# Optimization experiments

Measured on AMD Instinct MI355X. Metric: run time of the kernel, lower is better.

Reference implementation:

```python
import jax, jax.numpy as jnp
import numpy as np

T, B, E, H = 256, 8, 512, 32
EXP = 512            # number of expanded (periodic-image) keys
SMOOTH = 20.0        # smooth_factor


def setup_inputs() -> dict:
    key = jax.random.key(0)
    ks = jax.random.split(key, 12)
    s = 1.0 / np.sqrt(E)
    return {
        "query": jax.random.normal(ks[0], (T, B, E), dtype=jnp.float32),
        "outcell_index": jax.random.randint(ks[1], (B, EXP), 0, T),
        "expand_mask": jax.random.bernoulli(ks[2], 0.1, (B, EXP)),
        "key_padding_mask": jax.random.bernoulli(ks[3], 0.1, (B, T)),
        "local_attention_weight": jax.random.uniform(ks[4], (B, T, T + EXP), dtype=jnp.float32),
        "Wq": jax.random.normal(ks[5], (E, E), dtype=jnp.float32) * s,
        "bq": jnp.zeros((E,), dtype=jnp.float32),
        "Wk": jax.random.normal(ks[6], (E, E), dtype=jnp.float32) * s,   # k_bias=False
        "Wv": jax.random.normal(ks[7], (E, E), dtype=jnp.float32) * s,
        "bv": jnp.zeros((E,), dtype=jnp.float32),
        "Wo": jax.random.normal(ks[8], (E, E), dtype=jnp.float32) * s,
        "bo": jnp.zeros((E,), dtype=jnp.float32),
    }


def reference(query, outcell_index, expand_mask, key_padding_mask,
              local_attention_weight, Wq, bq, Wk, Wv, bv, Wo, bo):
    t, b, e = query.shape
    hd = e // H
    # QKV projections (torch Linear: y = x @ W.T + b)
    q = jnp.einsum('tbe,fe->tbf', query, Wq) + bq
    k = jnp.einsum('tbe,fe->tbf', query, Wk)          # no k bias
    v = jnp.einsum('tbe,fe->tbf', query, Wv) + bv
    # PBC gather-expand K/V along the time axis
    oc = outcell_index.T[:, :, None]                  # [EXP, B, 1]
    k = jnp.concatenate([k, jnp.take_along_axis(k, oc, axis=0)], axis=0)  # [S,B,E]
    v = jnp.concatenate([v, jnp.take_along_axis(v, oc, axis=0)], axis=0)
    s_len = k.shape[0]
    # [len, B, E] -> [B, H, len, hd]
    qh = q.reshape(t, b, H, hd).transpose(1, 2, 0, 3)
    kh = k.reshape(s_len, b, H, hd).transpose(1, 2, 0, 3)
    vh = v.reshape(s_len, b, H, hd).transpose(1, 2, 0, 3)
    # NOTE: forward() never applies self.scaling in this path (faithful)
    scores = jnp.einsum('bhtd,bhsd->bhts', qh, kh)    # [B,H,T,S]
    law = local_attention_weight[:, None]             # [B,1,T,S]
    scores = (scores + SMOOTH) * law - SMOOTH         # smooth softmax
    kpm = jnp.concatenate([key_padding_mask, expand_mask], axis=1)  # [B,S]
    scores = jnp.where(kpm[:, None, None, :], -jnp.inf, scores)
    probs = jax.nn.softmax(scores, axis=-1)
    probs = probs * law                               # post-softmax reweight
    attn = jnp.einsum('bhts,bhsd->bhtd', probs, vh)   # [B,H,T,hd]
    attn = attn.transpose(2, 0, 1, 3).reshape(t, b, e)
    return jnp.einsum('tbe,fe->tbf', attn, Wo) + bo
```

## Files before the change

kernel.cpp:

```cpp
#include <hip/hip_runtime.h>
#include <stdint.h>

#define T_ 256
#define B_ 8
#define E_ 512
#define H_ 32
#define HD_ 16
#define EXP_ 512
#define S_ 768
#define M_ 2048
#define SMOOTH_ 20.0f
#define VSTR 776
#define OSTR 20
#define LWSTR 36
#define LOG2E_ 1.44269504f
#define MB0_  (-100.988655f)

typedef __attribute__((ext_vector_type(8)))  short bf16x8;
typedef __attribute__((ext_vector_type(4)))  float f32x4;
typedef __attribute__((ext_vector_type(16))) float f32x16;
typedef __attribute__((ext_vector_type(2)))  unsigned int uint32x2;

__device__ __forceinline__ unsigned int pku(float a, float b)
{
    return ((__float_as_uint(a) + 0x8000u) >> 16) |
           ((__float_as_uint(b) + 0x8000u) & 0xFFFF0000u);
}
__device__ __forceinline__ ushort bf1(float a)
{
    unsigned int u = __float_as_uint(a);
    u = u + 0x7FFFu + ((u >> 16) & 1u);
    return (ushort)(u >> 16);
}

union U16 { uint4 u; bf16x8 v; };

__global__ __launch_bounds__(1024, 4)
void qkv_attn_kernel(const float* __restrict__ X,
                     const float* __restrict__ Wq, const float* __restrict__ Wk,
                     const float* __restrict__ Wv,
                     const float* __restrict__ bq, const float* __restrict__ bv,
                     const float* __restrict__ LAW,
                     const int* __restrict__ kpm, const int* __restrict__ em,
                     const int* __restrict__ oc, ushort* __restrict__ Ab)
{
    __shared__ __align__(16) char raw[134400];
    ushort* Ks  = (ushort*)(raw);
    ushort* Vt  = (ushort*)(raw + 24576);
    ushort* Qi  = (ushort*)(raw + 49408);
    float*  msf = (float*) (raw + 57600);
    float*  LAWf= (float*) (raw + 60672);
    ushort* As  = (ushort*)(raw);
    ushort* Bs  = (ushort*)(raw + 36864);
    float*  Obuf= (float*) (raw);
    float*  Zb  = (float*) (raw + 57600);
    ushort* Ob  = Qi;

    const int bh  = blockIdx.x;
    const int b   = bh & 7;
    const int h   = bh >> 3;
    const int tid = threadIdx.x;
    const int w   = tid >> 6;
    const int l   = tid & 63;

    const int r0 = tid >> 3;
    const int c8 = tid & 7;
    const float* Xc0 = &X[((size_t)r0 * 8 + b) * E_ + c8 * 8];
    const float* Xc1 = Xc0 + (size_t)128 * 8 * E_;

    const int wr = tid >> 3;
    const bool wload = (tid < 384);
    const float* Wsel = (wr < 16) ? Wq : (wr < 32 ? Wk : Wv);
    const float* Wr = &Wsel[((size_t)(h * 16 + (wr & 15))) * E_ + c8 * 8];
    ushort* Bxw = &Bs[wr * 72 + c8 * 8];

    f32x4 acc[3];
#pragma unroll
    for (int m = 0; m < 3; ++m) acc[m] = (f32x4){0.f, 0.f, 0.f, 0.f};

    float4 xa0, xa1, xb0, xb1, wp0, wp1;
    xa0 = *(const float4*)&Xc0[0]; xa1 = *(const float4*)&Xc0[4];
    xb0 = *(const float4*)&Xc1[0]; xb1 = *(const float4*)&Xc1[4];
    if (wload) { wp0 = *(const float4*)&Wr[0]; wp1 = *(const float4*)&Wr[4]; }

    const int ln = l & 15;
    const int lg = l >> 4;

    for (int it = 0; it < 8; ++it) {
        __syncthreads();
        *(uint4*)&As[r0 * 72 + c8 * 8] =
            make_uint4(pku(xa0.x, xa0.y), pku(xa0.z, xa0.w),
                       pku(xa1.x, xa1.y), pku(xa1.z, xa1.w));
        *(uint4*)&As[(r0 + 128) * 72 + c8 * 8] =
            make_uint4(pku(xb0.x, xb0.y), pku(xb0.z, xb0.w),
                       pku(xb1.x, xb1.y), pku(xb1.z, xb1.w));
        if (wload)
            *(uint4*)&Bxw[0] = make_uint4(pku(wp0.x, wp0.y), pku(wp0.z, wp0.w),
                                          pku(wp1.x, wp1.y), pku(wp1.z, wp1.w));
        __syncthreads();
        if (it < 7) {
            Xc0 += 64; Xc1 += 64;
            xa0 = *(const float4*)&Xc0[0]; xa1 = *(const float4*)&Xc0[4];
            xb0 = *(const float4*)&Xc1[0]; xb1 = *(const float4*)&Xc1[4];
            if (wload) { Wr += 64; wp0 = *(const float4*)&Wr[0]; wp1 = *(const float4*)&Wr[4]; }
        }
#pragma unroll
        for (int kb = 0; kb < 2; ++kb) {
            bf16x8 af = *(const bf16x8*)&As[(w * 16 + ln) * 72 + kb * 32 + lg * 8];
#pragma unroll
            for (int m = 0; m < 3; ++m) {
                bf16x8 bfm = *(const bf16x8*)&Bs[(m * 16 + ln) * 72 + kb * 32 + lg * 8];
                acc[m] = __builtin_amdgcn_mfma_f32_16x16x32_bf16(af, bfm, acc[m], 0, 0, 0);
            }
        }
    }

    __syncthreads();

    {
        const float bqv = bq[h * 16 + ln];
        const float bvv = bv[h * 16 + ln];
#pragma unroll
        for (int r = 0; r < 4; ++r) {
            const int t = w * 16 + lg * 4 + r;
            Qi[t * 16 + ln]   = bf1(acc[0][r] + bqv);
            Ks[t * 16 + ln]   = bf1(acc[1][r]);
            Vt[ln * VSTR + t] = bf1(acc[2][r] + bvv);
        }
    }

    const int tq = w & 7;
    const int sh = w >> 3;
    const int i0 = sh * 12;
    const int iend = i0 + 12;
    float* lws = &LAWf[w * 32 * LWSTR];
    const int srow = l >> 1;
    const int scol = (l & 1) * 16;
    const float* gl = &LAW[((size_t)b * T_ + tq * 32 + srow) * S_ + scol];

    float4 g0 = *(const float4*)&gl[i0 * 32 + 0];
    float4 g1 = *(const float4*)&gl[i0 * 32 + 4];
    float4 g2 = *(const float4*)&gl[i0 * 32 + 8];
    float4 g3 = *(const float4*)&gl[i0 * 32 + 12];
    *(float4*)&lws[srow * LWSTR + scol + 0]  = g0;
    *(float4*)&lws[srow * LWSTR + scol + 4]  = g1;
    *(float4*)&lws[srow * LWSTR + scol + 8]  = g2;
    *(float4*)&lws[srow * LWSTR + scol + 12] = g3;
    g0 = *(const float4*)&gl[(i0 + 1) * 32 + 0];
    g1 = *(const float4*)&gl[(i0 + 1) * 32 + 4];
    g2 = *(const float4*)&gl[(i0 + 1) * 32 + 8];
    g3 = *(const float4*)&gl[(i0 + 1) * 32 + 12];

    __syncthreads();

    if (tid < 512) {
        const int j   = tid;
        const int src = oc[b * EXP_ + j];
        uint4 k0 = *(const uint4*)&Ks[src * 16];
        uint4 k1 = *(const uint4*)&Ks[src * 16 + 8];
        *(uint4*)&Ks[(T_ + j) * 16]     = k0;
        *(uint4*)&Ks[(T_ + j) * 16 + 8] = k1;
    } else {
        const int j   = tid - 512;
        const int src = oc[b * EXP_ + j];
#pragma unroll
        for (int d = 0; d < 16; ++d)
            Vt[d * VSTR + T_ + j] = Vt[d * VSTR + src];
    }
    if (tid < 768) {
        const int s = tid;
        const int m = (s < T_) ? kpm[b * T_ + s] : em[b * EXP_ + (s - T_)];
        msf[s] = m ? -1.0e5f : MB0_;
    }
    __syncthreads();

    const int slane = l & 31;
    const int hi    = l >> 5;

    bf16x8 qf = *(const bf16x8*)&Qi[(tq * 32 + slane) * 16 + hi * 8];

    const f32x16 zero16 = {0.f,0.f,0.f,0.f,0.f,0.f,0.f,0.f,
                           0.f,0.f,0.f,0.f,0.f,0.f,0.f,0.f};
    f32x16 oacc = zero16;
    float z = 0.f;

    for (int i = i0; i < iend; ++i) {
        bf16x8 kf = *(const bf16x8*)&Ks[(i * 32 + slane) * 16 + hi * 8];
        f32x16 sc = __builtin_amdgcn_mfma_f32_32x32x16_bf16(kf, qf, zero16, 0, 0, 0);

#pragma unroll
        for (int ks = 0; ks < 2; ++ks) {
            float pp[8];
#pragma unroll
            for (int gi = 0; gi < 2; ++gi) {
                const int g = 2 * ks + gi;
                const float4 lw4 = *(const float4*)&lws[slane * LWSTR + g * 8 + 4 * hi];
                const float4 mb4 = *(const float4*)&msf[i * 32 + g * 8 + 4 * hi];
                const float lwa[4] = {lw4.x, lw4.y, lw4.z, lw4.w};
                const float mba[4] = {mb4.x, mb4.y, mb4.z, mb4.w};
#pragma unroll
                for (int c = 0; c < 4; ++c) {
                    const float lwv = lwa[c];
                    const float lwK = lwv * LOG2E_;
                    const float arg = __builtin_fmaf(sc[8 * ks + 4 * gi + c], lwK,
                                      __builtin_fmaf(lwK, SMOOTH_, mba[c]));
                    const float e = __builtin_amdgcn_exp2f(arg);
                    z += e;
                    pp[4 * gi + c] = e * lwv;
                }
            }
            const unsigned int cA0 = pku(pp[0], pp[1]);
            const unsigned int cA2 = pku(pp[2], pp[3]);
            const unsigned int cB0 = pku(pp[4], pp[5]);
            const unsigned int cB2 = pku(pp[6], pp[7]);
            uint32x2 s0 = __builtin_amdgcn_permlane32_swap(cA0, cB0, false, false);
            uint32x2 s1 = __builtin_amdgcn_permlane32_swap(cA2, cB2, false, false);
            U16 u;
            u.u = make_uint4(s0.x, s1.x, s0.y, s1.y);
            bf16x8 vf = *(const bf16x8*)&Vt[(l & 15) * VSTR + i * 32 + ks * 16 + hi * 8];
            oacc = __builtin_amdgcn_mfma_f32_32x32x16_bf16(u.v, vf, oacc, 0, 0, 0);
        }

        if (i + 1 < iend) {
            *(float4*)&lws[srow * LWSTR + scol + 0]  = g0;
            *(float4*)&lws[srow * LWSTR + scol + 4]  = g1;
            *(float4*)&lws[srow * LWSTR + scol + 8]  = g2;
            *(float4*)&lws[srow * LWSTR + scol + 12] = g3;
            if (i + 2 < iend) {
                g0 = *(const float4*)&gl[(i + 2) * 32 + 0];
                g1 = *(const float4*)&gl[(i + 2) * 32 + 4];
                g2 = *(const float4*)&gl[(i + 2) * 32 + 8];
                g3 = *(const float4*)&gl[(i + 2) * 32 + 12];
            }
        }
    }

    z += __shfl_xor(z, 32);

    __syncthreads();

    if (l < 32) Zb[sh * 256 + tq * 32 + l] = z;

    const int dl = l & 15;
    const bool dok = (l & 31) < 16;
    if (sh == 1 && dok) {
#pragma unroll
        for (int r = 0; r < 16; ++r) {
            const int t = tq * 32 + (r & 3) + 8 * (r >> 2) + 4 * hi;
            Obuf[t * OSTR + dl] = oacc[r];
        }
    }
    __syncthreads();

    if (sh == 0 && dok) {
#pragma unroll
        for (int r = 0; r < 16; ++r) {
            const int t = tq * 32 + (r & 3) + 8 * (r >> 2) + 4 * hi;
            const float Zt  = Zb[t] + Zb[256 + t];
            const float inv = (Zt > 0.f) ? 1.f / Zt : 0.f;
            const float ov  = (oacc[r] + Obuf[t * OSTR + dl]) * inv;
            Ob[t * 16 + dl] = bf1(ov);
        }
    }
    __syncthreads();

    {
        const int t  = tid >> 2;
        const int q4 = tid & 3;
        *(uint2*)&Ab[((size_t)(t * 8 + b)) * E_ + h * 16 + q4 * 4] =
            *(const uint2*)&Ob[t * 16 + q4 * 4];
    }
}

__global__ __launch_bounds__(256, 2)
void out_gemm(const ushort* __restrict__ Ab, const float* __restrict__ Wo,
              const float* __restrict__ bo, float* __restrict__ dst)
{
    __shared__ __align__(16) ushort sbuf[96 * 136];
    ushort* As = sbuf;
    ushort* Bs = sbuf + 32 * 136;

    const int n0 = blockIdx.x * 64;
    const int m0 = blockIdx.y * 32;

    const int tid = threadIdx.x;
    const int arow = tid >> 3;
    const int acol = (tid & 7) * 16;
    const int brow = tid >> 2;
    const int bcol = (tid & 3) * 32;

    const ushort* Ap = &Ab[(size_t)(m0 + arow) * E_ + acol];
    const float*  Wp = &Wo[(size_t)(n0 + brow) * E_ + bcol];

    f32x4 acc[2];
    acc[0] = (f32x4){0.f, 0.f, 0.f, 0.f};
    acc[1] = (f32x4){0.f, 0.f, 0.f, 0.f};

    uint4  ha0 = *(const uint4*)&Ap[0];
    uint4  ha1 = *(const uint4*)&Ap[8];
    float4 f0 = *(const float4*)&Wp[0];
    float4 f1 = *(const float4*)&Wp[4];
    float4 f2 = *(const float4*)&Wp[8];
    float4 f3 = *(const float4*)&Wp[12];
    float4 f4 = *(const float4*)&Wp[16];
    float4 f5 = *(const float4*)&Wp[20];
    float4 f6 = *(const float4*)&Wp[24];
    float4 f7 = *(const float4*)&Wp[28];

    const int l  = tid & 63;
    const int w  = tid >> 6;
    const int wm = w & 1;
    const int wn = w >> 1;
    const int lq = l >> 4;
    const int ln = l & 15;

    for (int it = 0; it < 4; ++it) {
        __syncthreads();
        *(uint4*)&As[arow * 136 + acol]     = ha0;
        *(uint4*)&As[arow * 136 + acol + 8] = ha1;
        *(uint4*)&Bs[brow * 136 + bcol]      = make_uint4(pku(f0.x, f0.y), pku(f0.z, f0.w),
                                                          pku(f1.x, f1.y), pku(f1.z, f1.w));
        *(uint4*)&Bs[brow * 136 + bcol + 8]  = make_uint4(pku(f2.x, f2.y), pku(f2.z, f2.w),
                                                          pku(f3.x, f3.y), pku(f3.z, f3.w));
        *(uint4*)&Bs[brow * 136 + bcol + 16] = make_uint4(pku(f4.x, f4.y), pku(f4.z, f4.w),
                                                          pku(f5.x, f5.y), pku(f5.z, f5.w));
        *(uint4*)&Bs[brow * 136 + bcol + 24] = make_uint4(pku(f6.x, f6.y), pku(f6.z, f6.w),
                                                          pku(f7.x, f7.y), pku(f7.z, f7.w));
        __syncthreads();
        if (it < 3) {
            Ap += 128; Wp += 128;
            ha0 = *(const uint4*)&Ap[0];
            ha1 = *(const uint4*)&Ap[8];
            f0 = *(const float4*)&Wp[0];
            f1 = *(const float4*)&Wp[4];
            f2 = *(const float4*)&Wp[8];
            f3 = *(const float4*)&Wp[12];
            f4 = *(const float4*)&Wp[16];
            f5 = *(const float4*)&Wp[20];
            f6 = *(const float4*)&Wp[24];
            f7 = *(const float4*)&Wp[28];
        }
#pragma unroll
        for (int kb = 0; kb < 4; ++kb) {
            bf16x8 af  = *(const bf16x8*)&As[(wm * 16 + ln) * 136 + kb * 32 + lq * 8];
            bf16x8 bv0 = *(const bf16x8*)&Bs[(wn * 32 + ln) * 136 + kb * 32 + lq * 8];
            bf16x8 bv1 = *(const bf16x8*)&Bs[(wn * 32 + 16 + ln) * 136 + kb * 32 + lq * 8];
            acc[0] = __builtin_amdgcn_mfma_f32_16x16x32_bf16(af, bv0, acc[0], 0, 0, 0);
            acc[1] = __builtin_amdgcn_mfma_f32_16x16x32_bf16(af, bv1, acc[1], 0, 0, 0);
        }
    }

    const float bo0 = bo[n0 + wn * 32 + ln];
    const float bo1 = bo[n0 + wn * 32 + 16 + ln];

    __syncthreads();
    float* Lf = (float*)sbuf;
#pragma unroll
    for (int j = 0; j < 2; ++j) {
        const float bb = j ? bo1 : bo0;
        const f32x4 a = acc[j];
#pragma unroll
        for (int r = 0; r < 4; ++r)
            Lf[(wm * 16 + lq * 4 + r) * 68 + wn * 32 + j * 16 + ln] = a[r] + bb;
    }
    __syncthreads();

    {
        const int orow = tid >> 3;
        const int oc8  = (tid & 7) * 8;
        float* dp = &dst[(size_t)(m0 + orow) * E_ + n0 + oc8];
        float4 v0 = *(const float4*)&Lf[orow * 68 + oc8];
        float4 v1 = *(const float4*)&Lf[orow * 68 + oc8 + 4];
        *(float4*)&dp[0] = v0;
        *(float4*)&dp[4] = v1;
    }
}

extern "C" void kernel_launch(void* const* d_in, const int* in_sizes, int n_in,
                              void* d_out, int out_size, void* d_ws, size_t ws_size,
                              hipStream_t stream)
{
    const float* query = (const float*)d_in[0];
    const int*   oc    = (const int*)d_in[1];
    const int*   em    = (const int*)d_in[2];
    const int*   kpm   = (const int*)d_in[3];
    const float* law   = (const float*)d_in[4];
    const float* Wq    = (const float*)d_in[5];
    const float* bq    = (const float*)d_in[6];
    const float* Wk    = (const float*)d_in[7];
    const float* Wv    = (const float*)d_in[8];
    const float* bv    = (const float*)d_in[9];
    const float* Wo    = (const float*)d_in[10];
    const float* bo    = (const float*)d_in[11];
    float* out = (float*)d_out;

    ushort* Ab = (ushort*)d_ws;

    qkv_attn_kernel<<<B_ * H_, 1024, 0, stream>>>(query, Wq, Wk, Wv, bq, bv,
                                                  law, kpm, em, oc, Ab);

    dim3 go(E_ / 64, M_ / 32, 1);
    out_gemm<<<go, 256, 0, stream>>>(Ab, Wo, bo, out);
}
```

Measured before the change: 125.3 us.

## Double-buffer QKV GEMM, load LAW directly to registers, pad K rows, use hardware bf16 convert

The QKV projection loop now alternates between two LDS buffers, which removes one barrier per iteration. Local attention weights are read straight from global memory into registers with a one-step prefetch, so the LDS staging buffer for them is gone and shared memory shrinks from about 134KB to about 88KB. K and Q rows are padded to stride 20 to reduce bank conflicts and read with split 8-byte loads. The next K fragment, V and the mask are prefetched, and softmax sums are split into four partial accumulators. Pack-to-bf16 now uses the v_cvt_pk_bf16_f32 instruction, which rounds to nearest-even, so results may differ slightly from the old truncating pack.

```diff
diff --git a/kernel.cpp b/kernel.cpp
--- a/kernel.cpp
+++ b/kernel.cpp
@@ -10,9 +10,9 @@
 #define S_ 768
 #define M_ 2048
 #define SMOOTH_ 20.0f
+#define KSTR 20
 #define VSTR 776
 #define OSTR 20
-#define LWSTR 36
 #define LOG2E_ 1.44269504f
 #define MB0_  (-100.988655f)
 
@@ -21,10 +21,11 @@
 typedef __attribute__((ext_vector_type(16))) float f32x16;
 typedef __attribute__((ext_vector_type(2)))  unsigned int uint32x2;
 
-__device__ __forceinline__ unsigned int pku(float a, float b)
-{
-    return ((__float_as_uint(a) + 0x8000u) >> 16) |
-           ((__float_as_uint(b) + 0x8000u) & 0xFFFF0000u);
+__device__ __forceinline__ unsigned int cvtpk(float a, float b)
+{
+    unsigned int r;
+    asm("v_cvt_pk_bf16_f32 %0, %1, %2" : "=v"(r) : "v"(a), "v"(b));
+    return r;
 }
 __device__ __forceinline__ ushort bf1(float a)
 {
@@ -34,6 +35,16 @@
 }
 
 union U16 { uint4 u; bf16x8 v; };
+union U8x2 { uint2 p[2]; bf16x8 v; };
+
+__device__ __forceinline__ bf16x8 ld20(const ushort* base, int row, int hi)
+{
+    U8x2 u;
+    const ushort* p = &base[row * KSTR + hi * 8];
+    u.p[0] = *(const uint2*)(p);
+    u.p[1] = *(const uint2*)(p + 4);
+    return u.v;
+}
 
 __global__ __launch_bounds__(1024, 4)
 void qkv_attn_kernel(const float* __restrict__ X,
@@ -44,16 +55,13 @@
                      const int* __restrict__ kpm, const int* __restrict__ em,
                      const int* __restrict__ oc, ushort* __restrict__ Ab)
 {
-    __shared__ __align__(16) char raw[134400];
+    __shared__ __align__(16) char raw[87552];
     ushort* Ks  = (ushort*)(raw);
-    ushort* Vt  = (ushort*)(raw + 24576);
-    ushort* Qi  = (ushort*)(raw + 49408);
-    float*  msf = (float*) (raw + 57600);
-    float*  LAWf= (float*) (raw + 60672);
-    ushort* As  = (ushort*)(raw);
-    ushort* Bs  = (ushort*)(raw + 36864);
+    ushort* Vt  = (ushort*)(raw + 30720);
+    ushort* Qi  = (ushort*)(raw + 55552);
+    float*  msf = (float*) (raw + 65792);
     float*  Obuf= (float*) (raw);
-    float*  Zb  = (float*) (raw + 57600);
+    float*  Zb  = (float*) (raw + 65792);
     ushort* Ob  = Qi;
 
     const int bh  = blockIdx.x;
@@ -72,7 +80,6 @@
     const bool wload = (tid < 384);
     const float* Wsel = (wr < 16) ? Wq : (wr < 32 ? Wk : Wv);
     const float* Wr = &Wsel[((size_t)(h * 16 + (wr & 15))) * E_ + c8 * 8];
-    ushort* Bxw = &Bs[wr * 72 + c8 * 8];
 
     f32x4 acc[3];
 #pragma unroll
@@ -87,16 +94,18 @@
     const int lg = l >> 4;
 
     for (int it = 0; it < 8; ++it) {
-        __syncthreads();
-        *(uint4*)&As[r0 * 72 + c8 * 8] =
-            make_uint4(pku(xa0.x, xa0.y), pku(xa0.z, xa0.w),
-                       pku(xa1.x, xa1.y), pku(xa1.z, xa1.w));
-        *(uint4*)&As[(r0 + 128) * 72 + c8 * 8] =
-            make_uint4(pku(xb0.x, xb0.y), pku(xb0.z, xb0.w),
-                       pku(xb1.x, xb1.y), pku(xb1.z, xb1.w));
+        ushort* Ad = (ushort*)(raw + (it & 1) * 43776);
+        ushort* Bd = Ad + 18432;
+        *(uint4*)&Ad[r0 * 72 + c8 * 8] =
+            make_uint4(cvtpk(xa0.x, xa0.y), cvtpk(xa0.z, xa0.w),
+                       cvtpk(xa1.x, xa1.y), cvtpk(xa1.z, xa1.w));
+        *(uint4*)&Ad[(r0 + 128) * 72 + c8 * 8] =
+            make_uint4(cvtpk(xb0.x, xb0.y), cvtpk(xb0.z, xb0.w),
+                       cvtpk(xb1.x, xb1.y), cvtpk(xb1.z, xb1.w));
         if (wload)
-            *(uint4*)&Bxw[0] = make_uint4(pku(wp0.x, wp0.y), pku(wp0.z, wp0.w),
-                                          pku(wp1.x, wp1.y), pku(wp1.z, wp1.w));
+            *(uint4*)&Bd[wr * 72 + c8 * 8] =
+                make_uint4(cvtpk(wp0.x, wp0.y), cvtpk(wp0.z, wp0.w),
+                           cvtpk(wp1.x, wp1.y), cvtpk(wp1.z, wp1.w));
         __syncthreads();
         if (it < 7) {
             Xc0 += 64; Xc1 += 64;
@@ -106,10 +115,10 @@
         }
 #pragma unroll
         for (int kb = 0; kb < 2; ++kb) {
-            bf16x8 af = *(const bf16x8*)&As[(w * 16 + ln) * 72 + kb * 32 + lg * 8];
+            bf16x8 af = *(const bf16x8*)&Ad[(w * 16 + ln) * 72 + kb * 32 + lg * 8];
 #pragma unroll
             for (int m = 0; m < 3; ++m) {
-                bf16x8 bfm = *(const bf16x8*)&Bs[(m * 16 + ln) * 72 + kb * 32 + lg * 8];
+                bf16x8 bfm = *(const bf16x8*)&Bd[(m * 16 + ln) * 72 + kb * 32 + lg * 8];
                 acc[m] = __builtin_amdgcn_mfma_f32_16x16x32_bf16(af, bfm, acc[m], 0, 0, 0);
             }
         }
@@ -123,43 +132,28 @@
 #pragma unroll
         for (int r = 0; r < 4; ++r) {
             const int t = w * 16 + lg * 4 + r;
-            Qi[t * 16 + ln]   = bf1(acc[0][r] + bqv);
-            Ks[t * 16 + ln]   = bf1(acc[1][r]);
+            Qi[t * KSTR + ln] = bf1(acc[0][r] + bqv);
+            Ks[t * KSTR + ln] = bf1(acc[1][r]);
             Vt[ln * VSTR + t] = bf1(acc[2][r] + bvv);
         }
     }
-
-    const int tq = w & 7;
-    const int sh = w >> 3;
-    const int i0 = sh * 12;
-    const int iend = i0 + 12;
-    float* lws = &LAWf[w * 32 * LWSTR];
-    const int srow = l >> 1;
-    const int scol = (l & 1) * 16;
-    const float* gl = &LAW[((size_t)b * T_ + tq * 32 + srow) * S_ + scol];
-
-    float4 g0 = *(const float4*)&gl[i0 * 32 + 0];
-    float4 g1 = *(const float4*)&gl[i0 * 32 + 4];
-    float4 g2 = *(const float4*)&gl[i0 * 32 + 8];
-    float4 g3 = *(const float4*)&gl[i0 * 32 + 12];
-    *(float4*)&lws[srow * LWSTR + scol + 0]  = g0;
-    *(float4*)&lws[srow * LWSTR + scol + 4]  = g1;
-    *(float4*)&lws[srow * LWSTR + scol + 8]  = g2;
-    *(float4*)&lws[srow * LWSTR + scol + 12] = g3;
-    g0 = *(const float4*)&gl[(i0 + 1) * 32 + 0];
-    g1 = *(const float4*)&gl[(i0 + 1) * 32 + 4];
-    g2 = *(const float4*)&gl[(i0 + 1) * 32 + 8];
-    g3 = *(const float4*)&gl[(i0 + 1) * 32 + 12];
-
     __syncthreads();
 
     if (tid < 512) {
         const int j   = tid;
         const int src = oc[b * EXP_ + j];
-        uint4 k0 = *(const uint4*)&Ks[src * 16];
-        uint4 k1 = *(const uint4*)&Ks[src * 16 + 8];
-        *(uint4*)&Ks[(T_ + j) * 16]     = k0;
-        *(uint4*)&Ks[(T_ + j) * 16 + 8] = k1;
+        const ushort* sp = &Ks[src * KSTR];
+        ushort* dp = &Ks[(T_ + j) * KSTR];
+        uint2 k0 = *(const uint2*)(sp);
+        uint2 k1 = *(const uint2*)(sp + 4);
+        uint2 k2 = *(const uint2*)(sp + 8);
+        uint2 k3 = *(const uint2*)(sp + 12);
+        uint2 k4 = *(const uint2*)(sp + 16);
+        *(uint2*)(dp)      = k0;
+        *(uint2*)(dp + 4)  = k1;
+        *(uint2*)(dp + 8)  = k2;
+        *(uint2*)(dp + 12) = k3;
+        *(uint2*)(dp + 16) = k4;
     } else {
         const int j   = tid - 512;
         const int src = oc[b * EXP_ + j];
@@ -176,17 +170,43 @@
 
     const int slane = l & 31;
     const int hi    = l >> 5;
-
-    bf16x8 qf = *(const bf16x8*)&Qi[(tq * 32 + slane) * 16 + hi * 8];
+    const int tq    = w & 7;
+    const int sh    = w >> 3;
+    const int i0    = sh * 12;
+    const int iend  = i0 + 12;
+
+    bf16x8 qf = ld20(Qi, tq * 32 + slane, hi);
 
     const f32x16 zero16 = {0.f,0.f,0.f,0.f,0.f,0.f,0.f,0.f,
                            0.f,0.f,0.f,0.f,0.f,0.f,0.f,0.f};
     f32x16 oacc = zero16;
-    float z = 0.f;
-
+    float zp0 = 0.f, zp1 = 0.f, zp2 = 0.f, zp3 = 0.f;
+
+    const float* lawb = &LAW[((size_t)b * T_ + tq * 32 + slane) * S_ + 4 * hi];
+
+    bf16x8 kf = ld20(Ks, i0 * 32 + slane, hi);
+    float4 g0 = *(const float4*)&lawb[i0 * 32];
+    float4 g1 = *(const float4*)&lawb[i0 * 32 + 8];
+    float4 g2 = *(const float4*)&lawb[i0 * 32 + 16];
+    float4 g3 = *(const float4*)&lawb[i0 * 32 + 24];
+
+#pragma unroll 2
     for (int i = i0; i < iend; ++i) {
-        bf16x8 kf = *(const bf16x8*)&Ks[(i * 32 + slane) * 16 + hi * 8];
+        const int inx = (i + 1 < iend) ? (i + 1) : i0;
+
+        bf16x8 vf0 = *(const bf16x8*)&Vt[(l & 15) * VSTR + i * 32 + hi * 8];
+        bf16x8 vf1 = *(const bf16x8*)&Vt[(l & 15) * VSTR + i * 32 + 16 + hi * 8];
+        const float4 m0 = *(const float4*)&msf[i * 32 + 4 * hi];
+        const float4 m1 = *(const float4*)&msf[i * 32 + 8 + 4 * hi];
+        const float4 m2 = *(const float4*)&msf[i * 32 + 16 + 4 * hi];
+        const float4 m3 = *(const float4*)&msf[i * 32 + 24 + 4 * hi];
+
         f32x16 sc = __builtin_amdgcn_mfma_f32_32x32x16_bf16(kf, qf, zero16, 0, 0, 0);
+
+        bf16x8 kfn = ld20(Ks, inx * 32 + slane, hi);
+
+        const float4 lwg[4] = {g0, g1, g2, g3};
+        const float4 mbg[4] = {m0, m1, m2, m3};
 
 #pragma unroll
         for (int ks = 0; ks < 2; ++ks) {
@@ -194,8 +214,8 @@
 #pragma unroll
             for (int gi = 0; gi < 2; ++gi) {
                 const int g = 2 * ks + gi;
-                const float4 lw4 = *(const float4*)&lws[slane * LWSTR + g * 8 + 4 * hi];
-                const float4 mb4 = *(const float4*)&msf[i * 32 + g * 8 + 4 * hi];
+                const float4 lw4 = lwg[g];
+                const float4 mb4 = mbg[g];
                 const float lwa[4] = {lw4.x, lw4.y, lw4.z, lw4.w};
                 const float mba[4] = {mb4.x, mb4.y, mb4.z, mb4.w};
 #pragma unroll
@@ -205,36 +225,31 @@
                     const float arg = __builtin_fmaf(sc[8 * ks + 4 * gi + c], lwK,
                                       __builtin_fmaf(lwK, SMOOTH_, mba[c]));
                     const float e = __builtin_amdgcn_exp2f(arg);
-                    z += e;
+                    if (c == 0) zp0 += e; else if (c == 1) zp1 += e;
+                    else if (c == 2) zp2 += e; else zp3 += e;
                     pp[4 * gi + c] = e * lwv;
                 }
             }
-            const unsigned int cA0 = pku(pp[0], pp[1]);
-            const unsigned int cA2 = pku(pp[2], pp[3]);
-            const unsigned int cB0 = pku(pp[4], pp[5]);
-            const unsigned int cB2 = pku(pp[6], pp[7]);
+            const unsigned int cA0 = cvtpk(pp[0], pp[1]);
+            const unsigned int cA2 = cvtpk(pp[2], pp[3]);
+            const unsigned int cB0 = cvtpk(pp[4], pp[5]);
+            const unsigned int cB2 = cvtpk(pp[6], pp[7]);
             uint32x2 s0 = __builtin_amdgcn_permlane32_swap(cA0, cB0, false, false);
             uint32x2 s1 = __builtin_amdgcn_permlane32_swap(cA2, cB2, false, false);
             U16 u;
             u.u = make_uint4(s0.x, s1.x, s0.y, s1.y);
-            bf16x8 vf = *(const bf16x8*)&Vt[(l & 15) * VSTR + i * 32 + ks * 16 + hi * 8];
-            oacc = __builtin_amdgcn_mfma_f32_32x32x16_bf16(u.v, vf, oacc, 0, 0, 0);
-        }
-
-        if (i + 1 < iend) {
-            *(float4*)&lws[srow * LWSTR + scol + 0]  = g0;
-            *(float4*)&lws[srow * LWSTR + scol + 4]  = g1;
-            *(float4*)&lws[srow * LWSTR + scol + 8]  = g2;
-            *(float4*)&lws[srow * LWSTR + scol + 12] = g3;
-            if (i + 2 < iend) {
-                g0 = *(const float4*)&gl[(i + 2) * 32 + 0];
-                g1 = *(const float4*)&gl[(i + 2) * 32 + 4];
-                g2 = *(const float4*)&gl[(i + 2) * 32 + 8];
-                g3 = *(const float4*)&gl[(i + 2) * 32 + 12];
-            }
-        }
-    }
-
+            oacc = __builtin_amdgcn_mfma_f32_32x32x16_bf16(
+                       u.v, ks ? vf1 : vf0, oacc, 0, 0, 0);
+        }
+
+        g0 = *(const float4*)&lawb[inx * 32];
+        g1 = *(const float4*)&lawb[inx * 32 + 8];
+        g2 = *(const float4*)&lawb[inx * 32 + 16];
+        g3 = *(const float4*)&lawb[inx * 32 + 24];
+        kf = kfn;
+    }
+
+    float z = (zp0 + zp1) + (zp2 + zp3);
     z += __shfl_xor(z, 32);
 
     __syncthreads();
@@ -318,14 +333,14 @@
         __syncthreads();
         *(uint4*)&As[arow * 136 + acol]     = ha0;
         *(uint4*)&As[arow * 136 + acol + 8] = ha1;
-        *(uint4*)&Bs[brow * 136 + bcol]      = make_uint4(pku(f0.x, f0.y), pku(f0.z, f0.w),
-                                                          pku(f1.x, f1.y), pku(f1.z, f1.w));
-        *(uint4*)&Bs[brow * 136 + bcol + 8]  = make_uint4(pku(f2.x, f2.y), pku(f2.z, f2.w),
-                                                          pku(f3.x, f3.y), pku(f3.z, f3.w));
-        *(uint4*)&Bs[brow * 136 + bcol + 16] = make_uint4(pku(f4.x, f4.y), pku(f4.z, f4.w),
-                                                          pku(f5.x, f5.y), pku(f5.z, f5.w));
-        *(uint4*)&Bs[brow * 136 + bcol + 24] = make_uint4(pku(f6.x, f6.y), pku(f6.z, f6.w),
-                                                          pku(f7.x, f7.y), pku(f7.z, f7.w));
+        *(uint4*)&Bs[brow * 136 + bcol]      = make_uint4(cvtpk(f0.x, f0.y), cvtpk(f0.z, f0.w),
+                                                          cvtpk(f1.x, f1.y), cvtpk(f1.z, f1.w));
+        *(uint4*)&Bs[brow * 136 + bcol + 8]  = make_uint4(cvtpk(f2.x, f2.y), cvtpk(f2.z, f2.w),
+                                                          cvtpk(f3.x, f3.y), cvtpk(f3.z, f3.w));
+        *(uint4*)&Bs[brow * 136 + bcol + 16] = make_uint4(cvtpk(f4.x, f4.y), cvtpk(f4.z, f4.w),
+                                                          cvtpk(f5.x, f5.y), cvtpk(f5.z, f5.w));
+        *(uint4*)&Bs[brow * 136 + bcol + 24] = make_uint4(cvtpk(f6.x, f6.y), cvtpk(f6.z, f6.w),
+                                                          cvtpk(f7.x, f7.y), cvtpk(f7.z, f7.w));
         __syncthreads();
         if (it < 3) {
             Ap += 128; Wp += 128;
```

New measurement: 131.1 us. 4.6% more time.
